# Kernel tuning notes

Measured on AMD Instinct MI355X. Metric: run time of the kernel, lower is better.

The kernel has to match this reference:

```python
import jax, jax.numpy as jnp
import numpy as np

N = 2048      # nodes
E = 65536     # edges (avg degree 32)
IN_C = 512
OUT_C = 512
KP1 = 3       # K=2 Chebyshev -> 3 terms


def setup_inputs() -> dict:
    key = jax.random.key(0)
    k0, k1, k2, k3, k4 = jax.random.split(key, 5)
    X_real = jax.random.normal(k0, (N, IN_C), jnp.float32)
    X_imag = jax.random.normal(k1, (N, IN_C), jnp.float32)
    edges = jax.random.randint(k2, (2, E), 0, N).astype(jnp.int64)
    edge_weight = jax.random.uniform(k3, (E,), jnp.float32)
    q = jnp.float32(0.25)
    stdv = 1.0 / np.sqrt(OUT_C)
    weight = jax.random.uniform(k4, (KP1, IN_C, OUT_C), jnp.float32, -stdv, stdv)
    bias = jnp.zeros((1, OUT_C), jnp.float32)
    return {"X_real": X_real, "X_imag": X_imag, "edges": edges, "q": q,
            "edge_weight": edge_weight, "weight": weight, "bias": bias}


def _cheb_laplacians(edges, edge_weight, q):
    """QinDirect_hermitian_decomp_sparse (norm=True, laplacian=True, max_eigen=2,
    gcn_appr=False) followed by cheb_poly_sparse with K=2. Returns stacked
    real/imag parts of [T0, T1, T2], each [KP1, N, N]."""
    f, e = edges[0], edges[1]
    A = jnp.zeros((N, N), jnp.float32).at[f, e].add(edge_weight)
    A_sym = 0.5 * (A + A.T)
    deg = A_sym.sum(axis=0)
    dinv = jnp.where(deg == 0.0, 1.0, deg) ** -0.5
    A_norm = dinv[:, None] * A_sym * dinv[None, :]   # D^-1/2 A_sym D^-1/2
    theta = (2.0 * jnp.pi) * q * (A - A.T)           # phase matrix
    # L = I - exp(i*theta) .* A_norm ; scaled (2/max_eigen)*L - I with max_eigen=2
    # => L_scaled = -exp(i*theta) .* A_norm
    L1_re = -jnp.cos(theta) * A_norm
    L1_im = -jnp.sin(theta) * A_norm
    eye = jnp.eye(N, dtype=jnp.float32)
    # T2 = 2*L1@L1 - I (complex square in real arithmetic)
    L2_re = 2.0 * (L1_re @ L1_re - L1_im @ L1_im) - eye
    L2_im = 2.0 * (L1_re @ L1_im + L1_im @ L1_re)
    L_re = jnp.stack([eye, L1_re, L2_re])                        # [KP1,N,N]
    L_im = jnp.stack([jnp.zeros((N, N), jnp.float32), L1_im, L2_im])
    return L_re, L_im


def reference(X_real, X_imag, edges, q, edge_weight, weight, bias):
    L_re, L_im = _cheb_laplacians(edges, edge_weight, q)
    # NOTE: original forward swaps the lists: L_norm_real = L_img, L_norm_imag = L_real.
    mr, mi = L_im, L_re
    # per term k: real_k = (mr_k@Xr - mi_k@Xi) @ W_k ; imag_k = (mi_k@Xr + mr_k@Xi) @ W_k
    Ar = jnp.einsum('knm,mf->knf', mr, X_real) - jnp.einsum('knm,mf->knf', mi, X_imag)
    Ai = jnp.einsum('knm,mf->knf', mi, X_real) + jnp.einsum('knm,mf->knf', mr, X_imag)
    real = jnp.einsum('knf,kfo->no', Ar, weight)   # sum over K terms
    imag = jnp.einsum('knf,kfo->no', Ai, weight)
    return real + bias, imag + bias
```

## Files before the change

kernel.cpp:

```cpp
#include <hip/hip_runtime.h>
#include <hip/hip_bf16.h>
#include <math.h>

#define NN 2048
#define CC 512
#define NEDGE 65536

typedef __hip_bfloat16 bf16;
typedef __attribute__((ext_vector_type(8))) short short8;
typedef __attribute__((ext_vector_type(4))) float floatx4;

static constexpr float TWO_PI_F = 6.2831853071795864769f;

__device__ __forceinline__ void gld16(const void* g, void* l) {
    __builtin_amdgcn_global_load_lds(
        (const __attribute__((address_space(1))) unsigned int*)(unsigned long long)(uintptr_t)g,
        (__attribute__((address_space(3))) unsigned int*)(unsigned long long)(uintptr_t)l,
        16, 0, 0);
}

__global__ __launch_bounds__(256) void detect_k(const unsigned int* __restrict__ qword,
                                                const unsigned int* __restrict__ ewords,
                                                int* __restrict__ flag,
                                                float* __restrict__ colsum) {
    int tid = threadIdx.x;
#pragma unroll
    for (int i = 0; i < 8; ++i) colsum[tid * 8 + i] = 0.f;
    if (tid < 64) {
        unsigned int w0 = ewords[2 * tid + 1];
        unsigned int w1 = ewords[128 + 2 * tid + 1];
        unsigned long long b = __ballot((w0 | w1) != 0u);
        if (tid == 0) {
            flag[0] = ((qword[0] & 0xFFFFu) == 0x3E80u) ? 1 : 0;
            flag[1] = (b == 0ull) ? 1 : 0;
        }
    }
}


__global__ void scatter_edges_k(const void* __restrict__ edges,
                                const void* __restrict__ w,
                                float* __restrict__ A,
                                const int* __restrict__ flag) {
    int e = blockIdx.x * 256 + threadIdx.x;
    if (e >= NEDGE) return;
    int f, t;
    if (flag[1]) {
        f = (int)((const long long*)edges)[e];
        t = (int)((const long long*)edges)[NEDGE + e];
    } else {
        f = ((const int*)edges)[e];
        t = ((const int*)edges)[NEDGE + e];
    }
    float wv = flag[0] ? __bfloat162float(((const bf16*)w)[e]) : ((const float*)w)[e];
    f &= (NN - 1); t &= (NN - 1);
    atomicAdd(&A[(size_t)f * NN + t], wv);
}

__global__ void row_sums_k(const float* __restrict__ A, float* __restrict__ rowsum) {
    int i = blockIdx.x;
    float s = 0.f;
    for (int j = threadIdx.x; j < NN; j += 256) s += A[(size_t)i * NN + j];
    __shared__ float red[256];
    red[threadIdx.x] = s;
    __syncthreads();
    for (int off = 128; off > 0; off >>= 1) {
        if (threadIdx.x < off) red[threadIdx.x] += red[threadIdx.x + off];
        __syncthreads();
    }
    if (threadIdx.x == 0) rowsum[i] = red[0];
}

__global__ void col_sums_k(const float* __restrict__ A, float* __restrict__ colsum) {
    int col = blockIdx.x * 256 + threadIdx.x;
    int r0 = blockIdx.y * 64;
    float s = 0.f;
    for (int r = r0; r < r0 + 64; ++r) s += A[(size_t)r * NN + col];
    atomicAdd(&colsum[col], s);
}

__global__ __launch_bounds__(1024) void build_Mpack_k(
    const float* __restrict__ A,
    const float* __restrict__ rowsum, const float* __restrict__ colsum,
    const void* __restrict__ qp, bf16* __restrict__ Mpack,
    const int* __restrict__ flag) {
    __shared__ float tmir[32][33];
    int tx = threadIdx.x, ty = threadIdx.y;
    int j0 = blockIdx.x * 32, i0 = blockIdx.y * 32;
    tmir[ty][tx] = A[(size_t)(j0 + ty) * NN + i0 + tx];
    __syncthreads();
    int i = i0 + ty, j = j0 + tx;
    float qv = flag[0] ? __bfloat162float(((const bf16*)qp)[0]) : ((const float*)qp)[0];
    float di = 0.5f * (rowsum[i] + colsum[i]); di = (di == 0.f) ? 1.f : di;
    float dj = 0.5f * (rowsum[j] + colsum[j]); dj = (dj == 0.f) ? 1.f : dj;
    float a = A[(size_t)i * NN + j];
    float b = tmir[tx][ty];
    float an = rsqrtf(di) * (0.5f * (a + b)) * rsqrtf(dj);
    float th = TWO_PI_F * qv * (a - b);
    float sn, cs;
    sincosf(th, &sn, &cs);
    Mpack[(size_t)i * (2 * NN) + j]      = __float2bfloat16(-cs * an);
    Mpack[(size_t)i * (2 * NN) + NN + j] = __float2bfloat16(sn * an);
}

__global__ __launch_bounds__(1024) void convert_X_BT_k(
    const void* __restrict__ xr, const void* __restrict__ xi,
    bf16* __restrict__ Af, bf16* __restrict__ BT,
    const int* __restrict__ flag) {
    __shared__ float tr[32][33];
    __shared__ float ti[32][33];
    int tx = threadIdx.x, ty = threadIdx.y;
    int c0 = blockIdx.x * 32, r0 = blockIdx.y * 32;
    size_t sidx = (size_t)(r0 + ty) * CC + c0 + tx;
    float fr, fi;
    if (flag[0]) {
        fr = __bfloat162float(((const bf16*)xr)[sidx]);
        fi = __bfloat162float(((const bf16*)xi)[sidx]);
    } else {
        fr = ((const float*)xr)[sidx];
        fi = ((const float*)xi)[sidx];
    }
    int r = r0 + ty, c = c0 + tx;
    Af[(size_t)r * 1536 + c]        = __float2bfloat16(-fi);
    Af[(size_t)(NN + r) * 1536 + c] = __float2bfloat16(fr);
    tr[ty][tx] = fr;
    ti[ty][tx] = fi;
    __syncthreads();
    float xrt = tr[tx][ty];
    float xit = ti[tx][ty];
    int n = c0 + ty, k = r0 + tx;
    BT[(size_t)n * 4096 + k]                = __float2bfloat16(xrt);
    BT[(size_t)(512 + n) * 4096 + k]        = __float2bfloat16(xit);
    BT[(size_t)n * 4096 + 2048 + k]         = __float2bfloat16(-xit);
    BT[(size_t)(512 + n) * 4096 + 2048 + k] = __float2bfloat16(xrt);
}

__global__ __launch_bounds__(1024) void pack_WT_k(const void* __restrict__ Wt,
                                                  bf16* __restrict__ WT,
                                                  const int* __restrict__ flag) {
    __shared__ float lds[32][33];
    int tx = threadIdx.x, ty = threadIdx.y;
    int k0 = blockIdx.x * 32, o0 = blockIdx.y * 32;
    size_t sidx = (size_t)(k0 + ty) * CC + o0 + tx;
    lds[ty][tx] = flag[0] ? __bfloat162float(((const bf16*)Wt)[sidx])
                          : ((const float*)Wt)[sidx];
    __syncthreads();
    WT[(size_t)(o0 + ty) * 1536 + k0 + tx] = __float2bfloat16(lds[tx][ty]);
}

__global__ __launch_bounds__(1024) void packPT_k(const bf16* __restrict__ Pb,
                                                 bf16* __restrict__ BT,
                                                 bf16* __restrict__ Af) {
    __shared__ float t1[32][33];
    __shared__ float t2[32][33];
    int tx = threadIdx.x, ty = threadIdx.y;
    int k0 = blockIdx.x * 32, n0 = blockIdx.y * 32;
    size_t i1 = (size_t)(n0 + ty) * 2048 + k0 + tx;
    size_t i2 = (size_t)(512 + n0 + ty) * 2048 + k0 + tx;
    float s1 = 0.f, s2 = 0.f;
#pragma unroll
    for (int z = 0; z < 4; ++z) {
        s1 += __bfloat162float(Pb[(size_t)z * 1024 * 2048 + i1]);
        s2 += __bfloat162float(Pb[(size_t)z * 1024 * 2048 + i2]);
    }
    t1[ty][tx] = s1;
    t2[ty][tx] = s2;
    BT[(size_t)(n0 + ty) * 4096 + k0 + tx]              = __float2bfloat16(s1);
    BT[(size_t)(n0 + ty) * 4096 + 2048 + k0 + tx]       = __float2bfloat16(-s2);
    BT[(size_t)(512 + n0 + ty) * 4096 + k0 + tx]        = __float2bfloat16(s2);
    BT[(size_t)(512 + n0 + ty) * 4096 + 2048 + k0 + tx] = __float2bfloat16(s1);
    __syncthreads();
    Af[(size_t)(k0 + ty) * 1536 + 512 + n0 + tx]        = __float2bfloat16(-t2[tx][ty]);
    Af[(size_t)(NN + k0 + ty) * 1536 + 512 + n0 + tx]   = __float2bfloat16(t1[tx][ty]);
}

__global__ void epi2_k(const bf16* __restrict__ Pb,
                       const void* __restrict__ xr, const void* __restrict__ xi,
                       bf16* __restrict__ Af, const int* __restrict__ flag) {
    int idx = blockIdx.x * 256 + threadIdx.x;
    if (idx >= NN * 1024) return;
    int r = idx >> 10, c = idx & 1023;
    float s = 0.f;
#pragma unroll
    for (int z = 0; z < 4; ++z)
        s += __bfloat162float(Pb[(size_t)z * NN * 1024 + idx]);
    size_t xoff = (size_t)r * CC + (c & (CC - 1));
    float xv;
    if (c < 512) xv = flag[0] ? __bfloat162float(((const bf16*)xr)[xoff]) : ((const float*)xr)[xoff];
    else         xv = flag[0] ? __bfloat162float(((const bf16*)xi)[xoff]) : ((const float*)xi)[xoff];
    float v = 2.f * s - xv;
    if (c < 512) Af[(size_t)(NN + r) * 1536 + 1024 + c] = __float2bfloat16(v);
    else         Af[(size_t)r * 1536 + 1024 + (c - 512)] = __float2bfloat16(-v);
}

__global__ void epi3_k(const bf16* __restrict__ Pb, const void* __restrict__ bias,
                       void* __restrict__ out, const int* __restrict__ flag) {
    int idx = blockIdx.x * 256 + threadIdx.x;
    if (idx >= 4096 * CC) return;
    int c = idx & (CC - 1);
    float s = 0.f;
#pragma unroll
    for (int z = 0; z < 4; ++z)
        s += __bfloat162float(Pb[(size_t)z * 4096 * CC + idx]);
    float bb = flag[0] ? __bfloat162float(((const bf16*)bias)[c]) : ((const float*)bias)[c];
    float o = s + bb;
    if (flag[0]) ((bf16*)out)[idx] = __float2bfloat16(o);
    else         ((float*)out)[idx] = o;
}

__global__ __launch_bounds__(256) void gemm_sk_k(
    const bf16* __restrict__ Ab, const bf16* __restrict__ BTb,
    int M, int N, int K, int klen,
    bf16* __restrict__ Pb)
{
    __shared__ bf16 sA[128 * 64];
    __shared__ bf16 sB[128 * 64];
    int tid = threadIdx.x;
    int w = tid >> 6, lane = tid & 63;
    int row0 = blockIdx.y * 128, col0 = blockIdx.x * 128;
    int kbase = blockIdx.z * klen;
    int wave_m = (w >> 1) * 64, wave_n = (w & 1) * 64;
    int lm = lane & 15, lq = lane >> 4;

    int srow = lane >> 3;
    int sg   = lane & 7;
    int scol = (sg ^ srow) * 8;
    const bf16 *gA[4], *gB[4];
    bf16 *lA[4], *lB[4];
#pragma unroll
    for (int i = 0; i < 4; ++i) {
        int c = w * 4 + i;
        int row = c * 8 + srow;
        gA[i] = Ab  + (size_t)(row0 + row) * K + kbase + scol;
        gB[i] = BTb + (size_t)(col0 + row) * K + kbase + scol;
        lA[i] = sA + c * 512 + lane * 8;
        lB[i] = sB + c * 512 + lane * 8;
    }

    floatx4 acc[4][4];
#pragma unroll
    for (int mf = 0; mf < 4; ++mf)
#pragma unroll
        for (int nf = 0; nf < 4; ++nf)
            acc[mf][nf] = (floatx4){0.f, 0.f, 0.f, 0.f};

    for (int kk = 0; kk < klen; kk += 64) {
        __syncthreads();
#pragma unroll
        for (int i = 0; i < 4; ++i) {
            gld16(gA[i] + kk, lA[i]);
            gld16(gB[i] + kk, lB[i]);
        }
        __syncthreads();
#pragma unroll
        for (int ks = 0; ks < 2; ++ks) {
            short8 af[4], bfv[4];
#pragma unroll
            for (int mf = 0; mf < 4; ++mf) {
                int row = wave_m + mf * 16 + lm;
                int g = (ks * 4 + lq) ^ (row & 7);
                af[mf] = *(const short8*)&sA[row * 64 + g * 8];
            }
#pragma unroll
            for (int nf = 0; nf < 4; ++nf) {
                int row = wave_n + nf * 16 + lm;
                int g = (ks * 4 + lq) ^ (row & 7);
                bfv[nf] = *(const short8*)&sB[row * 64 + g * 8];
            }
#pragma unroll
            for (int mf = 0; mf < 4; ++mf)
#pragma unroll
                for (int nf = 0; nf < 4; ++nf)
                    acc[mf][nf] = __builtin_amdgcn_mfma_f32_16x16x32_bf16(
                        af[mf], bfv[nf], acc[mf][nf], 0, 0, 0);
        }
    }

    bf16* slice = Pb + (size_t)blockIdx.z * M * N;
#pragma unroll
    for (int mf = 0; mf < 4; ++mf) {
#pragma unroll
        for (int nf = 0; nf < 4; ++nf) {
            int gcol = col0 + wave_n + nf * 16 + lm;
#pragma unroll
            for (int r = 0; r < 4; ++r) {
                int grow = row0 + wave_m + mf * 16 + lq * 4 + r;
                slice[(size_t)grow * N + gcol] = __float2bfloat16(acc[mf][nf][r]);
            }
        }
    }
}


extern "C" void kernel_launch(void* const* d_in, const int* in_sizes, int n_in,
                              void* d_out, int out_size, void* d_ws, size_t ws_size,
                              hipStream_t stream) {
    const void* Xr_in = d_in[0];
    const void* Xi_in = d_in[1];
    const void* edges = d_in[2];
    const void* q     = d_in[3];
    const void* ew    = d_in[4];
    const void* Wt    = d_in[5];
    const void* bias  = d_in[6];

    char* base = (char*)d_ws;
    const size_t MB = 1024 * 1024;
    float* A      = (float*)(base);
    bf16*  Pb     = (bf16*)(base);
    bf16*  Mpack  = (bf16*)(base + 16 * MB);
    bf16*  Af     = (bf16*)(base + 32 * MB);
    bf16*  BTb    = (bf16*)(base + 44 * MB);
    bf16*  WT     = (bf16*)(base + 52 * MB);
    float* rowsum = (float*)(base + 53 * MB + 512 * 1024);
    float* colsum = (float*)(base + 53 * MB + 520 * 1024);
    int*   flag   = (int*)  (base + 53 * MB + 528 * 1024);

    detect_k<<<1, 256, 0, stream>>>((const unsigned int*)q, (const unsigned int*)edges,
                                    flag, colsum);
    hipMemsetAsync(A, 0, 16 * MB, stream);

    scatter_edges_k<<<NEDGE / 256, 256, 0, stream>>>(edges, ew, A, flag);
    row_sums_k<<<NN, 256, 0, stream>>>(A, rowsum);
    col_sums_k<<<dim3(NN / 256, NN / 64), 256, 0, stream>>>(A, colsum);
    build_Mpack_k<<<dim3(NN / 32, NN / 32), dim3(32, 32), 0, stream>>>(
        A, rowsum, colsum, q, Mpack, flag);

    convert_X_BT_k<<<dim3(CC / 32, NN / 32), dim3(32, 32), 0, stream>>>(
        Xr_in, Xi_in, Af, BTb, flag);
    pack_WT_k<<<dim3(1536 / 32, CC / 32), dim3(32, 32), 0, stream>>>(Wt, WT, flag);

    gemm_sk_k<<<dim3(NN / 128, 1024 / 128, 4), 256, 0, stream>>>(
        BTb, Mpack, 1024, NN, 4096, 1024, Pb);
    packPT_k<<<dim3(2048 / 32, 512 / 32), dim3(32, 32), 0, stream>>>(Pb, BTb, Af);

    gemm_sk_k<<<dim3(1024 / 128, NN / 128, 4), 256, 0, stream>>>(
        Mpack, BTb, NN, 1024, 4096, 1024, Pb);
    epi2_k<<<(NN * 1024) / 256, 256, 0, stream>>>(Pb, Xr_in, Xi_in, Af, flag);

    gemm_sk_k<<<dim3(CC / 128, 4096 / 128, 4), 256, 0, stream>>>(
        Af, WT, 4096, CC, 1536, 384, Pb);
    epi3_k<<<(4096 * CC) / 256, 256, 0, stream>>>(Pb, bias, d_out, flag);
}
```

Measured before the change: 204.2 us.

## Merge row/col sums and input packing kernels; double split-K for big GEMMs

Merges the row-sum and column-sum kernels into one launch, and merges the X and W packing kernels into one launch, to cut launch overhead and let the pieces run together. The two large 2048x1024x4096 GEMMs move from 4-way to 8-way split-K, giving 1024 workgroups instead of 512 for better occupancy across CUs. The partial-sum buffer moves to its own workspace region so it no longer aliases A. In exchange, the reduction epilogues must read and sum twice as many bf16 partials.

```diff
diff --git a/kernel.cpp b/kernel.cpp
--- a/kernel.cpp
+++ b/kernel.cpp
@@ -57,26 +57,28 @@
     atomicAdd(&A[(size_t)f * NN + t], wv);
 }
 
-__global__ void row_sums_k(const float* __restrict__ A, float* __restrict__ rowsum) {
-    int i = blockIdx.x;
-    float s = 0.f;
-    for (int j = threadIdx.x; j < NN; j += 256) s += A[(size_t)i * NN + j];
-    __shared__ float red[256];
-    red[threadIdx.x] = s;
-    __syncthreads();
-    for (int off = 128; off > 0; off >>= 1) {
-        if (threadIdx.x < off) red[threadIdx.x] += red[threadIdx.x + off];
-        __syncthreads();
-    }
-    if (threadIdx.x == 0) rowsum[i] = red[0];
-}
-
-__global__ void col_sums_k(const float* __restrict__ A, float* __restrict__ colsum) {
-    int col = blockIdx.x * 256 + threadIdx.x;
-    int r0 = blockIdx.y * 64;
-    float s = 0.f;
-    for (int r = r0; r < r0 + 64; ++r) s += A[(size_t)r * NN + col];
-    atomicAdd(&colsum[col], s);
+__global__ void sums_k(const float* __restrict__ A,
+                       float* __restrict__ rowsum, float* __restrict__ colsum) {
+    int b = blockIdx.x;
+    if (b < NN) {
+        float s = 0.f;
+        for (int j = threadIdx.x; j < NN; j += 256) s += A[(size_t)b * NN + j];
+        __shared__ float red[256];
+        red[threadIdx.x] = s;
+        __syncthreads();
+        for (int off = 128; off > 0; off >>= 1) {
+            if (threadIdx.x < off) red[threadIdx.x] += red[threadIdx.x + off];
+            __syncthreads();
+        }
+        if (threadIdx.x == 0) rowsum[b] = red[0];
+    } else {
+        int bb = b - NN;
+        int col = (bb & 7) * 256 + threadIdx.x;
+        int r0 = (bb >> 3) * 64;
+        float s = 0.f;
+        for (int r = r0; r < r0 + 64; ++r) s += A[(size_t)r * NN + col];
+        atomicAdd(&colsum[col], s);
+    }
 }
 
 __global__ __launch_bounds__(1024) void build_Mpack_k(
@@ -103,49 +105,50 @@
     Mpack[(size_t)i * (2 * NN) + NN + j] = __float2bfloat16(sn * an);
 }
 
-__global__ __launch_bounds__(1024) void convert_X_BT_k(
+__global__ __launch_bounds__(1024) void pack_inputs_k(
     const void* __restrict__ xr, const void* __restrict__ xi,
-    bf16* __restrict__ Af, bf16* __restrict__ BT,
+    const void* __restrict__ Wt,
+    bf16* __restrict__ Af, bf16* __restrict__ BT, bf16* __restrict__ WT,
     const int* __restrict__ flag) {
-    __shared__ float tr[32][33];
-    __shared__ float ti[32][33];
-    int tx = threadIdx.x, ty = threadIdx.y;
-    int c0 = blockIdx.x * 32, r0 = blockIdx.y * 32;
-    size_t sidx = (size_t)(r0 + ty) * CC + c0 + tx;
-    float fr, fi;
-    if (flag[0]) {
-        fr = __bfloat162float(((const bf16*)xr)[sidx]);
-        fi = __bfloat162float(((const bf16*)xi)[sidx]);
+    __shared__ float t1[32][33];
+    __shared__ float t2[32][33];
+    int tid = threadIdx.x;
+    int tx = tid & 31, ty = tid >> 5;
+    int bx = blockIdx.x;
+    int isbf = flag[0];
+    if (bx < 1024) {
+        int c0 = (bx & 15) * 32, r0 = (bx >> 4) * 32;
+        size_t sidx = (size_t)(r0 + ty) * CC + c0 + tx;
+        float fr, fi;
+        if (isbf) {
+            fr = __bfloat162float(((const bf16*)xr)[sidx]);
+            fi = __bfloat162float(((const bf16*)xi)[sidx]);
+        } else {
+            fr = ((const float*)xr)[sidx];
+            fi = ((const float*)xi)[sidx];
+        }
+        int r = r0 + ty, c = c0 + tx;
+        Af[(size_t)r * 1536 + c]        = __float2bfloat16(-fi);
+        Af[(size_t)(NN + r) * 1536 + c] = __float2bfloat16(fr);
+        t1[ty][tx] = fr;
+        t2[ty][tx] = fi;
+        __syncthreads();
+        float xrt = t1[tx][ty];
+        float xit = t2[tx][ty];
+        int n = c0 + ty, k = r0 + tx;
+        BT[(size_t)n * 4096 + k]                = __float2bfloat16(xrt);
+        BT[(size_t)(512 + n) * 4096 + k]        = __float2bfloat16(xit);
+        BT[(size_t)n * 4096 + 2048 + k]         = __float2bfloat16(-xit);
+        BT[(size_t)(512 + n) * 4096 + 2048 + k] = __float2bfloat16(xrt);
     } else {
-        fr = ((const float*)xr)[sidx];
-        fi = ((const float*)xi)[sidx];
-    }
-    int r = r0 + ty, c = c0 + tx;
-    Af[(size_t)r * 1536 + c]        = __float2bfloat16(-fi);
-    Af[(size_t)(NN + r) * 1536 + c] = __float2bfloat16(fr);
-    tr[ty][tx] = fr;
-    ti[ty][tx] = fi;
-    __syncthreads();
-    float xrt = tr[tx][ty];
-    float xit = ti[tx][ty];
-    int n = c0 + ty, k = r0 + tx;
-    BT[(size_t)n * 4096 + k]                = __float2bfloat16(xrt);
-    BT[(size_t)(512 + n) * 4096 + k]        = __float2bfloat16(xit);
-    BT[(size_t)n * 4096 + 2048 + k]         = __float2bfloat16(-xit);
-    BT[(size_t)(512 + n) * 4096 + 2048 + k] = __float2bfloat16(xrt);
-}
-
-__global__ __launch_bounds__(1024) void pack_WT_k(const void* __restrict__ Wt,
-                                                  bf16* __restrict__ WT,
-                                                  const int* __restrict__ flag) {
-    __shared__ float lds[32][33];
-    int tx = threadIdx.x, ty = threadIdx.y;
-    int k0 = blockIdx.x * 32, o0 = blockIdx.y * 32;
-    size_t sidx = (size_t)(k0 + ty) * CC + o0 + tx;
-    lds[ty][tx] = flag[0] ? __bfloat162float(((const bf16*)Wt)[sidx])
+        int bw = bx - 1024;
+        int k0 = (bw % 48) * 32, o0 = (bw / 48) * 32;
+        size_t sidx = (size_t)(k0 + ty) * CC + o0 + tx;
+        t1[ty][tx] = isbf ? __bfloat162float(((const bf16*)Wt)[sidx])
                           : ((const float*)Wt)[sidx];
-    __syncthreads();
-    WT[(size_t)(o0 + ty) * 1536 + k0 + tx] = __float2bfloat16(lds[tx][ty]);
+        __syncthreads();
+        WT[(size_t)(o0 + ty) * 1536 + k0 + tx] = __float2bfloat16(t1[tx][ty]);
+    }
 }
 
 __global__ __launch_bounds__(1024) void packPT_k(const bf16* __restrict__ Pb,
@@ -159,7 +162,7 @@
     size_t i2 = (size_t)(512 + n0 + ty) * 2048 + k0 + tx;
     float s1 = 0.f, s2 = 0.f;
 #pragma unroll
-    for (int z = 0; z < 4; ++z) {
+    for (int z = 0; z < 8; ++z) {
         s1 += __bfloat162float(Pb[(size_t)z * 1024 * 2048 + i1]);
         s2 += __bfloat162float(Pb[(size_t)z * 1024 * 2048 + i2]);
     }
@@ -182,7 +185,7 @@
     int r = idx >> 10, c = idx & 1023;
     float s = 0.f;
 #pragma unroll
-    for (int z = 0; z < 4; ++z)
+    for (int z = 0; z < 8; ++z)
         s += __bfloat162float(Pb[(size_t)z * NN * 1024 + idx]);
     size_t xoff = (size_t)r * CC + (c & (CC - 1));
     float xv;
@@ -306,7 +309,6 @@
     char* base = (char*)d_ws;
     const size_t MB = 1024 * 1024;
     float* A      = (float*)(base);
-    bf16*  Pb     = (bf16*)(base);
     bf16*  Mpack  = (bf16*)(base + 16 * MB);
     bf16*  Af     = (bf16*)(base + 32 * MB);
     bf16*  BTb    = (bf16*)(base + 44 * MB);
@@ -314,27 +316,25 @@
     float* rowsum = (float*)(base + 53 * MB + 512 * 1024);
     float* colsum = (float*)(base + 53 * MB + 520 * 1024);
     int*   flag   = (int*)  (base + 53 * MB + 528 * 1024);
+    bf16*  Pb     = (bf16*)(base + 56 * MB);
 
     detect_k<<<1, 256, 0, stream>>>((const unsigned int*)q, (const unsigned int*)edges,
                                     flag, colsum);
     hipMemsetAsync(A, 0, 16 * MB, stream);
 
     scatter_edges_k<<<NEDGE / 256, 256, 0, stream>>>(edges, ew, A, flag);
-    row_sums_k<<<NN, 256, 0, stream>>>(A, rowsum);
-    col_sums_k<<<dim3(NN / 256, NN / 64), 256, 0, stream>>>(A, colsum);
+    sums_k<<<NN + 256, 256, 0, stream>>>(A, rowsum, colsum);
     build_Mpack_k<<<dim3(NN / 32, NN / 32), dim3(32, 32), 0, stream>>>(
         A, rowsum, colsum, q, Mpack, flag);
 
-    convert_X_BT_k<<<dim3(CC / 32, NN / 32), dim3(32, 32), 0, stream>>>(
-        Xr_in, Xi_in, Af, BTb, flag);
-    pack_WT_k<<<dim3(1536 / 32, CC / 32), dim3(32, 32), 0, stream>>>(Wt, WT, flag);
-
-    gemm_sk_k<<<dim3(NN / 128, 1024 / 128, 4), 256, 0, stream>>>(
-        BTb, Mpack, 1024, NN, 4096, 1024, Pb);
+    pack_inputs_k<<<1792, 1024, 0, stream>>>(Xr_in, Xi_in, Wt, Af, BTb, WT, flag);
+
+    gemm_sk_k<<<dim3(NN / 128, 1024 / 128, 8), 256, 0, stream>>>(
+        BTb, Mpack, 1024, NN, 4096, 512, Pb);
     packPT_k<<<dim3(2048 / 32, 512 / 32), dim3(32, 32), 0, stream>>>(Pb, BTb, Af);
 
-    gemm_sk_k<<<dim3(1024 / 128, NN / 128, 4), 256, 0, stream>>>(
-        Mpack, BTb, NN, 1024, 4096, 1024, Pb);
+    gemm_sk_k<<<dim3(1024 / 128, NN / 128, 8), 256, 0, stream>>>(
+        Mpack, BTb, NN, 1024, 4096, 512, Pb);
     epi2_k<<<(NN * 1024) / 256, 256, 0, stream>>>(Pb, Xr_in, Xi_in, Af, flag);
 
     gemm_sk_k<<<dim3(CC / 128, 4096 / 128, 4), 256, 0, stream>>>(
```

Measured after the change: 212.2 us. +3.9%, slower.
